# Kernel tuning notes

Measured on AMD Instinct MI355X. Metric: run time of the kernel, lower is better.

The kernel has to match this reference:

```python
import jax, jax.numpy as jnp
import numpy as np

D = 1024; H = 8; QLR = 384; KVLR = 256; NOPE = 128; ROPE = 64; VD = 128
E = 8; TOPK = 2; INTER = 512; NSH = 2; B = 2; T = 2048
QKD = NOPE + ROPE  # 192


def _rms(x, w, eps=1e-6):
    return x * jax.lax.rsqrt(jnp.mean(x * x, axis=-1, keepdims=True) + eps) * w


def _rope(x, cos, sin):
    # x: [B,T,h,ROPE]; pairs are consecutive elements (torch view(...,-1,2)).
    x0 = x[..., 0::2]
    x1 = x[..., 1::2]
    c = cos[None, :, None, :]
    s = sin[None, :, None, :]
    y0 = x0 * c - x1 * s
    y1 = x0 * s + x1 * c
    return jnp.stack([y0, y1], axis=-1).reshape(x.shape)


def setup_inputs() -> dict:
    key = jax.random.key(0)
    ks = jax.random.split(key, 12)
    def w(k, shape, scale=0.02):
        return jax.random.normal(k, shape, dtype=jnp.float32) * scale
    inv = 1.0 / (10000.0 ** (jnp.arange(0, ROPE, 2, dtype=jnp.float32) / ROPE))
    ang = jnp.arange(T, dtype=jnp.float32)[:, None] * inv[None, :]  # [T, ROPE//2]
    return {
        "x": jax.random.normal(ks[0], (B, T, D), dtype=jnp.float32),
        "freqs_cos": jnp.cos(ang),
        "freqs_sin": jnp.sin(ang),
        "rmsn1_w": jnp.ones((D,), jnp.float32),
        "rmsn2_w": jnp.ones((D,), jnp.float32),
        "latent_w": w(ks[1], (D, QLR + KVLR + ROPE)),
        "q_norm_w": jnp.ones((QLR,), jnp.float32),
        "q_up_w": w(ks[2], (QLR, H * QKD)),
        "kv_norm_w": jnp.ones((KVLR,), jnp.float32),
        "kv_up_w": w(ks[3], (KVLR, H * (NOPE + VD))),
        "c_proj_w": w(ks[4], (D, D)),
        "gate_w": w(ks[5], (D, E)),
        "sh_w1": w(ks[6], (D, INTER * NSH)),
        "sh_w2": w(ks[7], (INTER * NSH, D)),
        "sh_w3": w(ks[8], (D, INTER * NSH)),
        "e_w1": w(ks[9], (E, D, INTER)),
        "e_w2": w(ks[10], (E, INTER, D)),
        "e_w3": w(ks[11], (E, D, INTER)),
    }


def reference(x, freqs_cos, freqs_sin, rmsn1_w, rmsn2_w, latent_w, q_norm_w,
              q_up_w, kv_norm_w, kv_up_w, c_proj_w, gate_w, sh_w1, sh_w2,
              sh_w3, e_w1, e_w2, e_w3):
    Bx, Tx, _ = x.shape
    # ---- MLA attention ----
    h = _rms(x, rmsn1_w)
    lat = h @ latent_w
    q_l, kv_l, k_r = jnp.split(lat, [QLR, QLR + KVLR], axis=-1)
    q = (_rms(q_l, q_norm_w) @ q_up_w).reshape(Bx, Tx, H, QKD)
    q_n, q_r = q[..., :NOPE], q[..., NOPE:]
    q_r = _rope(q_r, freqs_cos, freqs_sin)
    q = jnp.concatenate([q_n, q_r], axis=-1)  # [B,T,H,QKD]
    kv = (_rms(kv_l, kv_norm_w) @ kv_up_w).reshape(Bx, Tx, H, NOPE + VD)
    k_n, v = kv[..., :NOPE], kv[..., NOPE:]
    k_r = _rope(k_r[:, :, None, :], freqs_cos, freqs_sin)
    k_r = jnp.broadcast_to(k_r, (Bx, Tx, H, ROPE))
    k = jnp.concatenate([k_n, k_r], axis=-1)
    scale = 1.0 / jnp.sqrt(jnp.float32(QKD))
    scores = jnp.einsum('bqhd,bkhd->bhqk', q, k) * scale
    causal = jnp.tril(jnp.ones((Tx, Tx), dtype=bool))
    scores = jnp.where(causal, scores, jnp.finfo(scores.dtype).min)
    attn = jax.nn.softmax(scores, axis=-1)
    y = jnp.einsum('bhqk,bkhd->bqhd', attn, v).reshape(Bx, Tx, D)
    x = x + y @ c_proj_w
    # ---- DeepSeekMoE ----
    h2 = _rms(x, rmsn2_w).reshape(-1, D)  # [N, D]
    y_sh = (jax.nn.silu(h2 @ sh_w1) * (h2 @ sh_w3)) @ sh_w2
    scores_g = jax.nn.softmax(h2 @ gate_w, axis=-1)  # [N, E]
    w_top, idx = jax.lax.top_k(scores_g, TOPK)  # weights == gathered original scores
    # combine weights per expert (route_scale = 1.0)
    cw = jnp.sum(jax.nn.one_hot(idx, E, dtype=h2.dtype) * w_top[..., None], axis=1)  # [N, E]
    h1 = jnp.einsum('nd,edi->eni', h2, e_w1)
    h3 = jnp.einsum('nd,edi->eni', h2, e_w3)
    out_e = jnp.einsum('eni,eid->end', jax.nn.silu(h1) * h3, e_w2)  # [E, N, D]
    y_moe = y_sh + jnp.einsum('end,ne->nd', out_e, cw)
    return x + y_moe.reshape(Bx, Tx, D)
```

## Files before the change

kernel.cpp:

```cpp
#include <hip/hip_runtime.h>
#include <hip/hip_bf16.h>
#include <math.h>

#define D_ 1024
#define H_ 8
#define QLR_ 384
#define KVLR_ 256
#define NOPE_ 128
#define ROPE_ 64
#define VD_ 128
#define E_ 8
#define INTER_ 512
#define B_ 2
#define T_ 2048
#define QKD_ 192
#define NTOK (B_*T_)
#define LSTR 4608
#define MAXMB 72

typedef __attribute__((ext_vector_type(8))) short short8;
typedef __attribute__((ext_vector_type(4))) float f32x4;
typedef __attribute__((ext_vector_type(4))) unsigned short us4;

__device__ __forceinline__ unsigned short f2bf(float f) {
  union { float f; unsigned u; } v; v.f = f;
  return (unsigned short)((v.u + 0x7FFFu + ((v.u >> 16) & 1u)) >> 16);
}
__device__ __forceinline__ float bf2f(unsigned short h) {
  union { unsigned u; float f; } v; v.u = ((unsigned)h) << 16;
  return v.f;
}

#define GLD16(SRC, DST) __builtin_amdgcn_global_load_lds( \
    (__attribute__((address_space(1))) void*)(SRC), \
    (__attribute__((address_space(3))) void*)(DST), 16, 0, 0)

#define DPPF(v, ctrl) __int_as_float(__builtin_amdgcn_update_dpp(0, __float_as_int(v), ctrl, 0xF, 0xF, true))
__device__ __forceinline__ float dppmax16(float v) {
  v = fmaxf(v, DPPF(v, 0xB1));
  v = fmaxf(v, DPPF(v, 0x4E));
  v = fmaxf(v, DPPF(v, 0x124));
  v = fmaxf(v, DPPF(v, 0x128));
  return v;
}
__device__ __forceinline__ float dppsum16(float v) {
  v += DPPF(v, 0xB1);
  v += DPPF(v, 0x4E);
  v += DPPF(v, 0x124);
  v += DPPF(v, 0x128);
  return v;
}

__global__ __launch_bounds__(256) void transpose_f32_bf16(
    const float* __restrict__ in, unsigned short* __restrict__ out,
    int R, int C, size_t inBS, size_t outBS) {
  __shared__ float tile[32][33];
  const float* inp = in + (size_t)blockIdx.z * inBS;
  unsigned short* outp = out + (size_t)blockIdx.z * outBS;
  int c0 = blockIdx.x * 32, r0 = blockIdx.y * 32;
  int tx = threadIdx.x & 31, ty = threadIdx.x >> 5;
  #pragma unroll
  for (int i = 0; i < 4; ++i) {
    int rr = ty + i * 8;
    tile[rr][tx] = inp[(size_t)(r0 + rr) * C + c0 + tx];
  }
  __syncthreads();
  #pragma unroll
  for (int i = 0; i < 4; ++i) {
    int rr = ty + i * 8;
    outp[(size_t)(c0 + rr) * R + r0 + tx] = f2bf(tile[tx][rr]);
  }
}

__global__ __launch_bounds__(256) void transpose_pair(
    const float* __restrict__ in1, const float* __restrict__ in3,
    unsigned short* __restrict__ out, int K, int C1, size_t inBS, size_t outBS) {
  __shared__ float tile[32][33];
  int z = blockIdx.z; int bat = z >> 1; int f = (z & 1) * 16;
  const float* src = ((z & 1) ? in3 : in1) + (size_t)bat * inBS;
  unsigned short* o = out + (size_t)bat * outBS;
  int c0 = blockIdx.x * 32, r0 = blockIdx.y * 32;
  int tx = threadIdx.x & 31, ty = threadIdx.x >> 5;
  #pragma unroll
  for (int i = 0; i < 4; ++i) {
    int rr = ty + i * 8;
    tile[rr][tx] = src[(size_t)(r0 + rr) * C1 + c0 + tx];
  }
  __syncthreads();
  #pragma unroll
  for (int i = 0; i < 4; ++i) {
    int cc = ty + i * 8;
    int c = c0 + cc;
    int n = ((c >> 4) << 5) + (c & 15) + f;
    o[(size_t)n * K + r0 + tx] = f2bf(tile[tx][cc]);
  }
}

template<typename TI>
__global__ __launch_bounds__(256) void rms_to_bf16(
    const TI* __restrict__ src, int stride, int off, const float* __restrict__ w,
    unsigned short* __restrict__ out, int Dd, int outStride) {
  int row = blockIdx.x;
  const TI* xr = src + (size_t)row * stride + off;
  float ss = 0.f;
  for (int i = threadIdx.x; i < Dd; i += 256) {
    float v;
    if constexpr (sizeof(TI) == 2) v = bf2f((unsigned short)xr[i]); else v = (float)xr[i];
    ss += v * v;
  }
  for (int o = 1; o < 64; o <<= 1) ss += __shfl_xor(ss, o);
  __shared__ float red[4];
  if ((threadIdx.x & 63) == 0) red[threadIdx.x >> 6] = ss;
  __syncthreads();
  float tot = red[0] + red[1] + red[2] + red[3];
  float inv = 1.f / sqrtf(tot / Dd + 1e-6f);
  for (int i = threadIdx.x; i < Dd; i += 256) {
    float v;
    if constexpr (sizeof(TI) == 2) v = bf2f((unsigned short)xr[i]); else v = (float)xr[i];
    out[(size_t)row * outStride + i] = f2bf(v * inv * w[i]);
  }
}

__global__ __launch_bounds__(256) void lat_post(
    const unsigned short* __restrict__ lat, const float* __restrict__ qw,
    const float* __restrict__ kw, const float* __restrict__ fc, const float* __restrict__ fs,
    unsigned short* __restrict__ qn, unsigned short* __restrict__ kvn,
    unsigned short* __restrict__ kr) {
  int row = blockIdx.x, tid = threadIdx.x;
  int lane = tid & 63, wv = tid >> 6;
  const unsigned short* lr = lat + (size_t)row * 768;
  float s1 = 0.f, s2 = 0.f;
  for (int i = tid; i < QLR_; i += 256) { float v = bf2f(lr[i]); s1 += v * v; }
  { float v = bf2f(lr[QLR_ + tid]); s2 = v * v; }
  for (int o = 1; o < 64; o <<= 1) { s1 += __shfl_xor(s1, o); s2 += __shfl_xor(s2, o); }
  __shared__ float red[8];
  if (lane == 0) { red[wv] = s1; red[4 + wv] = s2; }
  __syncthreads();
  float inv1 = 1.f / sqrtf((red[0] + red[1] + red[2] + red[3]) / QLR_ + 1e-6f);
  float inv2 = 1.f / sqrtf((red[4] + red[5] + red[6] + red[7]) / KVLR_ + 1e-6f);
  for (int i = tid; i < QLR_; i += 256)
    qn[(size_t)row * QLR_ + i] = f2bf(bf2f(lr[i]) * inv1 * qw[i]);
  kvn[(size_t)row * KVLR_ + tid] = f2bf(bf2f(lr[QLR_ + tid]) * inv2 * kw[tid]);
  if (tid < 32) {
    int t = row & (T_ - 1);
    float c = fc[t * 32 + tid], s = fs[t * 32 + tid];
    float x0 = bf2f(lr[640 + 2 * tid]), x1 = bf2f(lr[640 + 2 * tid + 1]);
    kr[(size_t)row * ROPE_ + 2 * tid]     = f2bf(x0 * c - x1 * s);
    kr[(size_t)row * ROPE_ + 2 * tid + 1] = f2bf(x0 * s + x1 * c);
  }
}

template<int MODE>
__global__ __launch_bounds__(256) void gemm_bf16(
    const unsigned short* __restrict__ A, const unsigned short* __restrict__ Bt,
    void* __restrict__ Cv, int M, int N, int K,
    const float* __restrict__ addv) {
  __shared__ __align__(16) unsigned short As[128 * 32];
  __shared__ __align__(16) unsigned short Bs[128 * 32];
  const int tid = threadIdx.x;
  const int lane = tid & 63, wave = tid >> 6;
  const int wm = wave >> 1, wn = wave & 1;
  const int bm = blockIdx.y * 128, bn = blockIdx.x * 128;
  const int r = lane & 15, g = lane >> 4;

  f32x4 acc[4][4];
  #pragma unroll
  for (int i = 0; i < 4; ++i)
    #pragma unroll
    for (int j = 0; j < 4; ++j) acc[i][j] = (f32x4)0.f;

  const int rl0 = wave * 16 + (lane >> 2);
  const int rl1 = rl0 + 64;
  const int kc = (lane & 3) * 8;
  char* AsB = (char*)As; char* BsB = (char*)Bs;

  for (int k0 = 0; k0 < K; k0 += 32) {
    GLD16(A + (size_t)(bm + rl0) * K + k0 + kc, AsB + wave * 1024);
    GLD16(A + (size_t)(bm + rl1) * K + k0 + kc, AsB + (wave + 4) * 1024);
    GLD16(Bt + (size_t)(bn + rl0) * K + k0 + kc, BsB + wave * 1024);
    GLD16(Bt + (size_t)(bn + rl1) * K + k0 + kc, BsB + (wave + 4) * 1024);
    __syncthreads();
    short8 af[4], bfr[4];
    #pragma unroll
    for (int mi = 0; mi < 4; ++mi)
      af[mi] = *(const short8*)(As + (wm * 64 + mi * 16 + r) * 32 + g * 8);
    #pragma unroll
    for (int nj = 0; nj < 4; ++nj)
      bfr[nj] = *(const short8*)(Bs + (wn * 64 + nj * 16 + r) * 32 + g * 8);
    #pragma unroll
    for (int mi = 0; mi < 4; ++mi)
      #pragma unroll
      for (int nj = 0; nj < 4; ++nj)
        acc[mi][nj] = __builtin_amdgcn_mfma_f32_16x16x32_bf16(af[mi], bfr[nj], acc[mi][nj], 0, 0, 0);
    __syncthreads();
  }

  const int orow0 = wm * 64 + g * 4;
  const int ocol0 = bn + wn * 64 + r;
  #pragma unroll
  for (int mi = 0; mi < 4; ++mi) {
    #pragma unroll
    for (int reg = 0; reg < 4; ++reg) {
      int mrow = bm + orow0 + mi * 16 + reg;
      size_t bas = (size_t)mrow * N + ocol0;
      if (MODE == 0) {
        unsigned short* C = (unsigned short*)Cv;
        #pragma unroll
        for (int nj = 0; nj < 4; ++nj) C[bas + nj * 16] = f2bf(acc[mi][nj][reg]);
      } else {
        float* C = (float*)Cv;
        #pragma unroll
        for (int nj = 0; nj < 4; ++nj) C[bas + nj * 16] = acc[mi][nj][reg] + addv[bas + nj * 16];
      }
    }
  }
}

__global__ __launch_bounds__(256) void gemm_qkv(
    const unsigned short* __restrict__ qn, const unsigned short* __restrict__ Wqup,
    const unsigned short* __restrict__ kvn, const unsigned short* __restrict__ Wkv,
    unsigned short* __restrict__ qq, unsigned short* __restrict__ kvb,
    unsigned short* __restrict__ vtg) {
  __shared__ __align__(16) unsigned short As[128 * 32];
  __shared__ __align__(16) unsigned short Bs[128 * 32];
  const int tid = threadIdx.x;
  const int lane = tid & 63, wave = tid >> 6;
  const int wm = wave >> 1, wn = wave & 1;
  const bool isQ = blockIdx.x < 12;
  const int bx = isQ ? blockIdx.x : blockIdx.x - 12;
  const unsigned short* A  = isQ ? qn : kvn;
  const unsigned short* Bt = isQ ? Wqup : Wkv;
  const int N = isQ ? 1536 : 2048;
  const int K = isQ ? QLR_ : KVLR_;
  const int bm = blockIdx.y * 128, bn = bx * 128;
  const int r = lane & 15, g = lane >> 4;

  f32x4 acc[4][4];
  #pragma unroll
  for (int i = 0; i < 4; ++i)
    #pragma unroll
    for (int j = 0; j < 4; ++j) acc[i][j] = (f32x4)0.f;

  const int rl0 = wave * 16 + (lane >> 2);
  const int rl1 = rl0 + 64;
  const int kc = (lane & 3) * 8;
  char* AsB = (char*)As; char* BsB = (char*)Bs;

  for (int k0 = 0; k0 < K; k0 += 32) {
    GLD16(A + (size_t)(bm + rl0) * K + k0 + kc, AsB + wave * 1024);
    GLD16(A + (size_t)(bm + rl1) * K + k0 + kc, AsB + (wave + 4) * 1024);
    GLD16(Bt + (size_t)(bn + rl0) * K + k0 + kc, BsB + wave * 1024);
    GLD16(Bt + (size_t)(bn + rl1) * K + k0 + kc, BsB + (wave + 4) * 1024);
    __syncthreads();
    short8 af[4], bfr[4];
    #pragma unroll
    for (int mi = 0; mi < 4; ++mi)
      af[mi] = *(const short8*)(As + (wm * 64 + mi * 16 + r) * 32 + g * 8);
    #pragma unroll
    for (int nj = 0; nj < 4; ++nj)
      bfr[nj] = *(const short8*)(Bs + (wn * 64 + nj * 16 + r) * 32 + g * 8);
    #pragma unroll
    for (int mi = 0; mi < 4; ++mi)
      #pragma unroll
      for (int nj = 0; nj < 4; ++nj)
        acc[mi][nj] = __builtin_amdgcn_mfma_f32_16x16x32_bf16(af[mi], bfr[nj], acc[mi][nj], 0, 0, 0);
    __syncthreads();
  }

  if (isQ) {
    const int orow0 = wm * 64 + g * 4;
    const int ocol0 = bn + wn * 64 + r;
    #pragma unroll
    for (int mi = 0; mi < 4; ++mi)
      #pragma unroll
      for (int reg = 0; reg < 4; ++reg) {
        int mrow = bm + orow0 + mi * 16 + reg;
        size_t bas = (size_t)mrow * 1536 + ocol0;
        #pragma unroll
        for (int nj = 0; nj < 4; ++nj) qq[bas + nj * 16] = f2bf(acc[mi][nj][reg]);
      }
  } else {
    const int colbase = bn + wn * 64;
    const int b = bm >> 11;
    const int hh = colbase >> 8;
    if ((colbase & 255) < 128) {
      #pragma unroll
      for (int mi = 0; mi < 4; ++mi)
        #pragma unroll
        for (int reg = 0; reg < 4; ++reg) {
          int mrow = bm + wm * 64 + mi * 16 + g * 4 + reg;
          size_t bas = (size_t)mrow * 2048 + colbase + r;
          #pragma unroll
          for (int nj = 0; nj < 4; ++nj) kvb[bas + nj * 16] = f2bf(acc[mi][nj][reg]);
        }
    } else {
      const int tl0 = (bm & 2047) + wm * 64 + g * 4;
      const int d0 = (colbase & 255) - 128 + r;
      const size_t bhbase = (size_t)(b * 8 + hh) * 64;
      #pragma unroll
      for (int mi = 0; mi < 4; ++mi) {
        int t = tl0 + mi * 16;
        size_t tb = (bhbase + (t >> 5)) * 4096 + (t & 31);
        #pragma unroll
        for (int nj = 0; nj < 4; ++nj) {
          int d = d0 + nj * 16;
          us4 pk;
          #pragma unroll
          for (int reg = 0; reg < 4; ++reg) pk[reg] = f2bf(acc[mi][nj][reg]);
          *(us4*)(vtg + tb + (size_t)d * 32) = pk;
        }
      }
    }
  }
}

__global__ __launch_bounds__(256) void gemm_ffn13(
    const unsigned short* __restrict__ h2b, const unsigned short* __restrict__ Wsh13,
    unsigned short* __restrict__ t1m,
    const unsigned short* __restrict__ Wew13, unsigned short* __restrict__ ehm,
    const int* __restrict__ lists, const int* __restrict__ map, const int* __restrict__ sbase) {
  __shared__ __align__(16) unsigned short As[128 * 32];
  __shared__ __align__(16) unsigned short Bs[128 * 32];
  const int i = blockIdx.x;
  const bool isSh = i < 512;
  const int tid = threadIdx.x, lane = tid & 63, wave = tid >> 6;
  const int wm = wave >> 1, wn = wave & 1;
  const int r = lane & 15, g = lane >> 4;
  const int rl0 = wave * 16 + (lane >> 2), rl1 = rl0 + 64;
  const int kc = (lane & 3) * 8;

  int bn, e = 0, ib = 0, bm = 0;
  const unsigned short* Bt;
  int ar0, ar1;
  const unsigned short* A;
  if (isSh) {
    bn = (i & 15) * 128; bm = (i >> 4) * 128;
    Bt = Wsh13; A = h2b;
    ar0 = bm + rl0; ar1 = bm + rl1;
  } else {
    int j = i - 512;
    bn = (j & 7) * 128;
    int mb = map[j >> 3];
    if (mb < 0) return;
    e = mb >> 16; ib = mb & 0xFFFF;
    Bt = Wew13 + (size_t)e * 1024 * 1024; A = h2b;
    ar0 = lists[e * LSTR + ib * 128 + rl0]; if (ar0 < 0) ar0 = 0;
    ar1 = lists[e * LSTR + ib * 128 + rl1]; if (ar1 < 0) ar1 = 0;
  }

  f32x4 acc[4][4];
  #pragma unroll
  for (int a = 0; a < 4; ++a)
    #pragma unroll
    for (int bj = 0; bj < 4; ++bj) acc[a][bj] = (f32x4)0.f;
  char* AsB = (char*)As; char* BsB = (char*)Bs;

  for (int k0 = 0; k0 < 1024; k0 += 32) {
    GLD16(A + (size_t)ar0 * 1024 + k0 + kc, AsB + wave * 1024);
    GLD16(A + (size_t)ar1 * 1024 + k0 + kc, AsB + (wave + 4) * 1024);
    GLD16(Bt + (size_t)(bn + rl0) * 1024 + k0 + kc, BsB + wave * 1024);
    GLD16(Bt + (size_t)(bn + rl1) * 1024 + k0 + kc, BsB + (wave + 4) * 1024);
    __syncthreads();
    short8 af[4], bfr[4];
    #pragma unroll
    for (int mi = 0; mi < 4; ++mi)
      af[mi] = *(const short8*)(As + (wm * 64 + mi * 16 + r) * 32 + g * 8);
    #pragma unroll
    for (int nj = 0; nj < 4; ++nj)
      bfr[nj] = *(const short8*)(Bs + (wn * 64 + nj * 16 + r) * 32 + g * 8);
    #pragma unroll
    for (int mi = 0; mi < 4; ++mi)
      #pragma unroll
      for (int nj = 0; nj < 4; ++nj)
        acc[mi][nj] = __builtin_amdgcn_mfma_f32_16x16x32_bf16(af[mi], bfr[nj], acc[mi][nj], 0, 0, 0);
    __syncthreads();
  }

  if (isSh) {
    const int hc = ((bn + wn * 64) >> 1) + r;
    #pragma unroll
    for (int mi = 0; mi < 4; ++mi)
      #pragma unroll
      for (int reg = 0; reg < 4; ++reg) {
        int mrow = bm + wm * 64 + mi * 16 + g * 4 + reg;
        #pragma unroll
        for (int p = 0; p < 2; ++p) {
          float a = acc[mi][2 * p][reg], b3 = acc[mi][2 * p + 1][reg];
          t1m[(size_t)mrow * 1024 + hc + p * 16] = f2bf((a / (1.f + __expf(-a))) * b3);
        }
      }
  } else {
    const int sb = sbase[e] + ib * 128;
    const int hc = ((bn + wn * 64) >> 1) + r;
    #pragma unroll
    for (int mi = 0; mi < 4; ++mi)
      #pragma unroll
      for (int reg = 0; reg < 4; ++reg) {
        int srow = sb + wm * 64 + mi * 16 + g * 4 + reg;
        #pragma unroll
        for (int p = 0; p < 2; ++p) {
          float a = acc[mi][2 * p][reg], b3 = acc[mi][2 * p + 1][reg];
          ehm[(size_t)srow * 512 + hc + p * 16] = f2bf((a / (1.f + __expf(-a))) * b3);
        }
      }
  }
}

__global__ __launch_bounds__(256) void gemm_ffn2(
    const unsigned short* __restrict__ t1m, const unsigned short* __restrict__ Wsh2,
    const unsigned short* __restrict__ ehm, const unsigned short* __restrict__ Wew2,
    float* __restrict__ out,
    const int* __restrict__ lists, const int* __restrict__ map, const int* __restrict__ sbase,
    const float* __restrict__ cw) {
  __shared__ __align__(16) unsigned short As[128 * 32];
  __shared__ __align__(16) unsigned short Bs[128 * 32];
  const int i = blockIdx.x;
  const bool isSh = i < 256;
  const int tid = threadIdx.x, lane = tid & 63, wave = tid >> 6;
  const int wm = wave >> 1, wn = wave & 1;
  const int r = lane & 15, g = lane >> 4;
  const int rl0 = wave * 16 + (lane >> 2), rl1 = rl0 + 64;
  const int kc = (lane & 3) * 8;

  int bn, e = 0, ib = 0, bm = 0, K, sb = 0;
  const unsigned short* A;
  const unsigned short* Bt;
  if (isSh) {
    bn = (i & 7) * 128; bm = (i >> 3) * 128;
    A = t1m; Bt = Wsh2; K = 1024;
  } else {
    int j = i - 256;
    bn = (j & 7) * 128;
    int mb = map[j >> 3];
    if (mb < 0) return;
    e = mb >> 16; ib = mb & 0xFFFF;
    sb = sbase[e] + ib * 128;
    A = ehm; Bt = Wew2 + (size_t)e * 512 * 1024; K = 512;
    bm = sb;
  }

  f32x4 acc[4][4];
  #pragma unroll
  for (int a = 0; a < 4; ++a)
    #pragma unroll
    for (int bj = 0; bj < 4; ++bj) acc[a][bj] = (f32x4)0.f;
  char* AsB = (char*)As; char* BsB = (char*)Bs;

  for (int k0 = 0; k0 < K; k0 += 32) {
    GLD16(A + (size_t)(bm + rl0) * K + k0 + kc, AsB + wave * 1024);
    GLD16(A + (size_t)(bm + rl1) * K + k0 + kc, AsB + (wave + 4) * 1024);
    GLD16(Bt + (size_t)(bn + rl0) * K + k0 + kc, BsB + wave * 1024);
    GLD16(Bt + (size_t)(bn + rl1) * K + k0 + kc, BsB + (wave + 4) * 1024);
    __syncthreads();
    short8 af[4], bfr[4];
    #pragma unroll
    for (int mi = 0; mi < 4; ++mi)
      af[mi] = *(const short8*)(As + (wm * 64 + mi * 16 + r) * 32 + g * 8);
    #pragma unroll
    for (int nj = 0; nj < 4; ++nj)
      bfr[nj] = *(const short8*)(Bs + (wn * 64 + nj * 16 + r) * 32 + g * 8);
    #pragma unroll
    for (int mi = 0; mi < 4; ++mi)
      #pragma unroll
      for (int nj = 0; nj < 4; ++nj)
        acc[mi][nj] = __builtin_amdgcn_mfma_f32_16x16x32_bf16(af[mi], bfr[nj], acc[mi][nj], 0, 0, 0);
    __syncthreads();
  }

  const int ocol0 = bn + wn * 64 + r;
  if (isSh) {
    #pragma unroll
    for (int mi = 0; mi < 4; ++mi)
      #pragma unroll
      for (int reg = 0; reg < 4; ++reg) {
        int mrow = bm + wm * 64 + mi * 16 + g * 4 + reg;
        #pragma unroll
        for (int nj = 0; nj < 4; ++nj)
          atomicAdd(out + (size_t)mrow * 1024 + ocol0 + nj * 16, acc[mi][nj][reg]);
      }
  } else {
    #pragma unroll
    for (int mi = 0; mi < 4; ++mi)
      #pragma unroll
      for (int reg = 0; reg < 4; ++reg) {
        int orow = wm * 64 + mi * 16 + g * 4 + reg;
        int tok = lists[e * LSTR + ib * 128 + orow];
        if (tok >= 0) {
          float wt = cw[(size_t)tok * E_ + e];
          #pragma unroll
          for (int nj = 0; nj < 4; ++nj)
            atomicAdd(out + (size_t)tok * 1024 + ocol0 + nj * 16, acc[mi][nj][reg] * wt);
        }
      }
  }
}

#define AQ 64
#define AK 32
#define VP 40
__global__ __launch_bounds__(256) void attn_mfma(
    const unsigned short* __restrict__ q,
    const unsigned short* __restrict__ kv,
    const unsigned short* __restrict__ kr,
    const unsigned short* __restrict__ vt,
    const float* __restrict__ fcos, const float* __restrict__ fsin,
    unsigned short* __restrict__ po,
    float* __restrict__ pml) {
  __shared__ __align__(16) unsigned short Ks[AK * 192];
  __shared__ __align__(16) unsigned short Vl[128 * VP];
  __shared__ __align__(16) unsigned short Ps[4 * 16 * VP];
  const int tid = threadIdx.x, lane = tid & 63, wave = tid >> 6;
  const int r = lane & 15, g = lane >> 4;
  const int bh = blockIdx.y, b = bh >> 3, h = bh & 7;
  const int qt = gridDim.x - 1 - blockIdx.x;
  const int q0 = qt * AQ;
  const int half = blockIdx.z;
  const int hnt = qt + 1;
  const int kb = half * hnt, ke = kb + hnt;
  const size_t bT = (size_t)b * T_;
  const unsigned short* vbase = vt + (size_t)bh * 64 * 4096;
  char* KsB = (char*)Ks;

  short8 qf[6];
  const int qrow = q0 + wave * 16 + r;
  {
    const unsigned short* qb = q + ((bT + qrow) * H_ + h) * 192;
    #pragma unroll
    for (int kk = 0; kk < 6; ++kk) qf[kk] = *(const short8*)(qb + kk * 32 + g * 8);
    #pragma unroll
    for (int kk = 4; kk < 6; ++kk) {
      int i0 = (kk - 4) * 16 + g * 4;
      #pragma unroll
      for (int p = 0; p < 4; ++p) {
        float cc = fcos[qrow * 32 + i0 + p], sn = fsin[qrow * 32 + i0 + p];
        float x0 = bf2f((unsigned short)qf[kk][2 * p]), x1 = bf2f((unsigned short)qf[kk][2 * p + 1]);
        qf[kk][2 * p]     = (short)f2bf(x0 * cc - x1 * sn);
        qf[kk][2 * p + 1] = (short)f2bf(x0 * sn + x1 * cc);
      }
    }
  }

  float m_i[4], l_i[4];
  f32x4 o[8];
  #pragma unroll
  for (int i = 0; i < 4; ++i) { m_i[i] = -1e30f; l_i[i] = 0.f; }
  #pragma unroll
  for (int cb = 0; cb < 8; ++cb) o[cb] = (f32x4)0.f;

  const float scale2 = 0.07216878364870322f * 1.44269504088896f;

  short8 kreg[3], vreg[2];
  int krow[3], kcol[3];
  #pragma unroll
  for (int it = 0; it < 3; ++it) {
    int c = tid + it * 256;
    krow[it] = c / 24; kcol[it] = c % 24;
    kreg[it] = (kcol[it] < 16)
      ? *(const short8*)(kv + ((bT + kb * AK + krow[it]) * H_ + h) * 256 + kcol[it] * 8)
      : *(const short8*)(kr + (bT + kb * AK + krow[it]) * 64 + (kcol[it] - 16) * 8);
  }
  #pragma unroll
  for (int it = 0; it < 2; ++it) {
    int x = tid + it * 256;
    vreg[it] = *(const short8*)(vbase + (size_t)kb * 4096 + x * 8);
  }

  for (int kt = kb; kt < ke; ++kt) {
    __builtin_amdgcn_s_barrier();
    __builtin_amdgcn_sched_barrier(0);
    #pragma unroll
    for (int it = 0; it < 3; ++it)
      *(short8*)(KsB + ((krow[it] * 384 + kcol[it] * 16) ^ ((krow[it] & 7) << 4))) = kreg[it];
    #pragma unroll
    for (int it = 0; it < 2; ++it) {
      int x = tid + it * 256;
      *(short8*)(Vl + (x >> 2) * VP + (x & 3) * 8) = vreg[it];
    }
    asm volatile("s_waitcnt lgkmcnt(0)" ::: "memory");
    __builtin_amdgcn_s_barrier();
    __builtin_amdgcn_sched_barrier(0);

    if (kt + 1 < ke) {
      int k1 = (kt + 1) * AK;
      #pragma unroll
      for (int it = 0; it < 3; ++it)
        kreg[it] = (kcol[it] < 16)
          ? *(const short8*)(kv + ((bT + k1 + krow[it]) * H_ + h) * 256 + kcol[it] * 8)
          : *(const short8*)(kr + (bT + k1 + krow[it]) * 64 + (kcol[it] - 16) * 8);
      #pragma unroll
      for (int it = 0; it < 2; ++it) {
        int x = tid + it * 256;
        vreg[it] = *(const short8*)(vbase + (size_t)(kt + 1) * 4096 + x * 8);
      }
    }

    const int k0 = kt * AK;
    f32x4 sf0 = (f32x4)0.f, sf1 = (f32x4)0.f;
    {
      int ksw = (r & 7) << 4;
      __builtin_amdgcn_s_setprio(1);
      #pragma unroll
      for (int kk = 0; kk < 6; ++kk) {
        short8 b0 = *(const short8*)(KsB + ((r * 384 + kk * 64 + g * 16) ^ ksw));
        short8 b1 = *(const short8*)(KsB + (((16 + r) * 384 + kk * 64 + g * 16) ^ ksw));
        sf0 = __builtin_amdgcn_mfma_f32_16x16x32_bf16(qf[kk], b0, sf0, 0, 0, 0);
        sf1 = __builtin_amdgcn_mfma_f32_16x16x32_bf16(qf[kk], b1, sf1, 0, 0, 0);
      }
      __builtin_amdgcn_s_setprio(0);
    }

    float fac[4];
    bool needs = false;
    const bool bnd = (k0 + AK > q0);
    #pragma unroll
    for (int reg = 0; reg < 4; ++reg) {
      float s0 = sf0[reg] * scale2;
      float s1 = sf1[reg] * scale2;
      if (bnd) {
        int qp = q0 + wave * 16 + g * 4 + reg;
        if (k0 + r > qp) s0 = -1e30f;
        if (k0 + 16 + r > qp) s1 = -1e30f;
      }
      float mt = dppmax16(fmaxf(s0, s1));
      float fc = 1.f, mn = m_i[reg];
      if (mt > mn + 8.f) {
        mn = mt; fc = exp2f(m_i[reg] - mn); m_i[reg] = mn; needs = true;
      }
      float e0 = exp2f(s0 - mn), e1 = exp2f(s1 - mn);
      float rs = dppsum16(e0 + e1);
      l_i[reg] = l_i[reg] * fc + rs;
      fac[reg] = fc;
      __hip_bfloat162 pk = __float22bfloat162_rn(float2{e0, e1});
      unsigned u = *(unsigned*)&pk;
      int prow = g * 4 + reg;
      Ps[wave * 16 * VP + prow * VP + r] = (unsigned short)u;
      Ps[wave * 16 * VP + prow * VP + 16 + r] = (unsigned short)(u >> 16);
    }
    if (__any(needs)) {
      #pragma unroll
      for (int cb = 0; cb < 8; ++cb)
        #pragma unroll
        for (int reg = 0; reg < 4; ++reg) o[cb][reg] *= fac[reg];
    }
    short8 pa = *(const short8*)(Ps + wave * 16 * VP + r * VP + g * 8);
    __builtin_amdgcn_s_setprio(1);
    #pragma unroll
    for (int cb = 0; cb < 8; ++cb) {
      short8 vb = *(const short8*)(Vl + (cb * 16 + r) * VP + g * 8);
      o[cb] = __builtin_amdgcn_mfma_f32_16x16x32_bf16(pa, vb, o[cb], 0, 0, 0);
    }
    __builtin_amdgcn_s_setprio(0);
  }

  const int slab = (bh * 32 + qt) * 2 + half;
  unsigned short* pob = po + (size_t)slab * 8192;
  float* pmlb = pml + (size_t)slab * 128;
  #pragma unroll
  for (int reg = 0; reg < 4; ++reg) {
    int row = wave * 16 + g * 4 + reg;
    if (r == 0) { pmlb[row * 2] = m_i[reg]; pmlb[row * 2 + 1] = l_i[reg]; }
    #pragma unroll
    for (int cb = 0; cb < 8; ++cb)
      pob[row * 128 + cb * 16 + r] = f2bf(o[cb][reg]);
  }
}

__global__ __launch_bounds__(256) void attn_combine(
    const unsigned short* __restrict__ po, const float* __restrict__ pml,
    unsigned short* __restrict__ y) {
  const int qt = blockIdx.x, bh = blockIdx.y, b = bh >> 3, h = bh & 7;
  const int s0 = (bh * 32 + qt) * 2, s1 = s0 + 1;
  const int row = threadIdx.x >> 2;
  const int qp = threadIdx.x & 3;
  float m0 = pml[(size_t)s0 * 128 + row * 2], l0 = pml[(size_t)s0 * 128 + row * 2 + 1];
  float m1 = pml[(size_t)s1 * 128 + row * 2], l1 = pml[(size_t)s1 * 128 + row * 2 + 1];
  float m = fmaxf(m0, m1);
  float e0 = exp2f(m0 - m), e1 = exp2f(m1 - m);
  float inv = 1.f / (l0 * e0 + l1 * e1);
  e0 *= inv; e1 *= inv;
  const unsigned short* o0 = po + (size_t)s0 * 8192 + row * 128 + qp * 32;
  const unsigned short* o1 = po + (size_t)s1 * 8192 + row * 128 + qp * 32;
  unsigned short* yb = y + ((size_t)(b * T_ + qt * 64 + row)) * 1024 + h * 128 + qp * 32;
  #pragma unroll
  for (int v = 0; v < 4; ++v) {
    short8 a = *(const short8*)(o0 + v * 8);
    short8 c = *(const short8*)(o1 + v * 8);
    short8 w;
    #pragma unroll
    for (int j = 0; j < 8; ++j)
      w[j] = (short)f2bf(bf2f((unsigned short)a[j]) * e0 + bf2f((unsigned short)c[j]) * e1);
    *(short8*)(yb + v * 8) = w;
  }
}

__global__ __launch_bounds__(256) void rms2_gate(
    const float* __restrict__ xo, const float* __restrict__ rw, const float* __restrict__ gw,
    unsigned short* __restrict__ h2b, float* __restrict__ cw) {
  int row = blockIdx.x, tid = threadIdx.x;
  int lane = tid & 63, wv = tid >> 6;
  const float* xr = xo + (size_t)row * D_;
  float v[4]; float ss = 0.f;
  #pragma unroll
  for (int j = 0; j < 4; ++j) { v[j] = xr[tid + j * 256]; ss += v[j] * v[j]; }
  for (int o = 1; o < 64; o <<= 1) ss += __shfl_xor(ss, o);
  __shared__ float red[4];
  if (lane == 0) red[wv] = ss;
  __syncthreads();
  float inv = 1.f / sqrtf((red[0] + red[1] + red[2] + red[3]) / D_ + 1e-6f);
  float a[E_] = {0, 0, 0, 0, 0, 0, 0, 0};
  #pragma unroll
  for (int j = 0; j < 4; ++j) {
    int i = tid + j * 256;
    float hv = v[j] * inv * rw[i];
    h2b[(size_t)row * D_ + i] = f2bf(hv);
    const float* wr = gw + (size_t)i * E_;
    #pragma unroll
    for (int e = 0; e < E_; ++e) a[e] += hv * wr[e];
  }
  #pragma unroll
  for (int e = 0; e < E_; ++e) {
    float t = a[e];
    for (int o = 1; o < 64; o <<= 1) t += __shfl_xor(t, o);
    a[e] = t;
  }
  __shared__ float ga[4][E_];
  if (lane == 0)
    #pragma unroll
    for (int e = 0; e < E_; ++e) ga[wv][e] = a[e];
  __syncthreads();
  if (tid == 0) {
    float lg[E_];
    #pragma unroll
    for (int e = 0; e < E_; ++e) lg[e] = ga[0][e] + ga[1][e] + ga[2][e] + ga[3][e];
    float mx = lg[0];
    #pragma unroll
    for (int e = 1; e < E_; ++e) mx = fmaxf(mx, lg[e]);
    float sum = 0.f; float p[E_];
    #pragma unroll
    for (int e = 0; e < E_; ++e) { p[e] = __expf(lg[e] - mx); sum += p[e]; }
    float is = 1.f / sum;
    int i1 = 0; float b1 = p[0];
    #pragma unroll
    for (int e = 1; e < E_; ++e) if (p[e] > b1) { b1 = p[e]; i1 = e; }
    int i2 = -1; float b2 = -1.f;
    #pragma unroll
    for (int e = 0; e < E_; ++e) if (e != i1 && p[e] > b2) { b2 = p[e]; i2 = e; }
    #pragma unroll
    for (int e = 0; e < E_; ++e)
      cw[(size_t)row * E_ + e] = (e == i1) ? b1 * is : (e == i2 ? b2 * is : 0.f);
  }
}

__global__ __launch_bounds__(256) void moe_build(const float* __restrict__ cw,
                                                 int* __restrict__ lists, int* __restrict__ counts) {
  int e = blockIdx.x, tid = threadIdx.x;
  int lane = tid & 63, wv = tid >> 6;
  __shared__ int wsum[4];
  __shared__ int base;
  if (tid == 0) base = 0;
  __syncthreads();
  for (int c0 = 0; c0 < NTOK; c0 += 256) {
    int tok = c0 + tid;
    bool f = cw[(size_t)tok * E_ + e] > 0.f;
    unsigned long long m = __ballot(f);
    int pos = __popcll(m & ((1ull << lane) - 1ull));
    if (lane == 0) wsum[wv] = __popcll(m);
    __syncthreads();
    int woff = base;
    #pragma unroll
    for (int w = 0; w < 4; ++w) if (w < wv) woff += wsum[w];
    if (f) lists[e * LSTR + woff + pos] = tok;
    __syncthreads();
    if (tid == 0) base += wsum[0] + wsum[1] + wsum[2] + wsum[3];
    __syncthreads();
  }
  int cnt = base;
  int padded = (cnt + 127) & ~127;
  for (int i2 = cnt + tid; i2 < padded; i2 += 256) lists[e * LSTR + i2] = -1;
  if (tid == 0) { counts[e] = cnt; counts[8 + e] = padded >> 7; }
}

__global__ void moe_finalize(const int* __restrict__ counts, int* __restrict__ map,
                             int* __restrict__ sbase) {
  if (threadIdx.x == 0 && blockIdx.x == 0) {
    int cum = 0;
    for (int e = 0; e < E_; ++e) {
      sbase[e] = cum * 128;
      int nb = counts[8 + e];
      for (int i = 0; i < nb; ++i) map[cum + i] = (e << 16) | i;
      cum += nb;
    }
    for (; cum < MAXMB; ++cum) map[cum] = -1;
  }
}

extern "C" void kernel_launch(void* const* d_in, const int* in_sizes, int n_in,
                              void* d_out, int out_size, void* d_ws, size_t ws_size,
                              hipStream_t stream) {
  const float* x        = (const float*)d_in[0];
  const float* fcos     = (const float*)d_in[1];
  const float* fsin     = (const float*)d_in[2];
  const float* rmsn1_w  = (const float*)d_in[3];
  const float* rmsn2_w  = (const float*)d_in[4];
  const float* latent_w = (const float*)d_in[5];
  const float* q_norm_w = (const float*)d_in[6];
  const float* q_up_w   = (const float*)d_in[7];
  const float* kv_norm_w= (const float*)d_in[8];
  const float* kv_up_w  = (const float*)d_in[9];
  const float* c_proj_w = (const float*)d_in[10];
  const float* gate_w   = (const float*)d_in[11];
  const float* sh_w1    = (const float*)d_in[12];
  const float* sh_w2    = (const float*)d_in[13];
  const float* sh_w3    = (const float*)d_in[14];
  const float* e_w1     = (const float*)d_in[15];
  const float* e_w2     = (const float*)d_in[16];
  const float* e_w3     = (const float*)d_in[17];
  float* out = (float*)d_out;

  char* base = (char*)d_ws;
  size_t off = 0;
  auto take = [&](size_t bytes) { char* p = base + off; off += (bytes + 255) & ~(size_t)255; return p; };
  unsigned short* Wlat  = (unsigned short*)take((size_t)768 * 1024 * 2);
  unsigned short* Wqup  = (unsigned short*)take((size_t)1536 * 384 * 2);
  unsigned short* Wkv   = (unsigned short*)take((size_t)2048 * 256 * 2);
  unsigned short* Wcp   = (unsigned short*)take((size_t)1024 * 1024 * 2);
  unsigned short* Wsh13 = (unsigned short*)take((size_t)2048 * 1024 * 2);
  unsigned short* Wsh2  = (unsigned short*)take((size_t)1024 * 1024 * 2);
  unsigned short* Wew13 = (unsigned short*)take((size_t)8 * 1024 * 1024 * 2);
  unsigned short* Wew2  = (unsigned short*)take((size_t)8 * 1024 * 512 * 2);
  float* cw             = (float*)take((size_t)NTOK * E_ * 4);
  int* lists            = (int*)take((size_t)E_ * LSTR * 4);
  int* counts           = (int*)take(64 * 4);
  int* map              = (int*)take(MAXMB * 4);
  int* sbase            = (int*)take(E_ * 4);
  unsigned short* Vtg   = (unsigned short*)take((size_t)16 * 64 * 4096 * 2);
  unsigned short* kr    = (unsigned short*)take((size_t)NTOK * 64 * 2);
  float* pml            = (float*)take((size_t)1024 * 128 * 4);

  size_t actStart = off;
  size_t aoff = actStart;
  auto takeA = [&](size_t bytes) { char* p = base + aoff; aoff += (bytes + 255) & ~(size_t)255; return p; };
  unsigned short* h_bf = (unsigned short*)takeA((size_t)NTOK * 1024 * 2);
  unsigned short* lat  = (unsigned short*)takeA((size_t)NTOK * 768 * 2);
  unsigned short* qn   = (unsigned short*)takeA((size_t)NTOK * 384 * 2);
  unsigned short* kvn  = (unsigned short*)takeA((size_t)NTOK * 256 * 2);
  unsigned short* qq   = (unsigned short*)takeA((size_t)NTOK * 1536 * 2);
  unsigned short* kvb  = (unsigned short*)takeA((size_t)NTOK * 2048 * 2);
  unsigned short* y    = (unsigned short*)takeA((size_t)NTOK * 1024 * 2);

  unsigned short* po   = (unsigned short*)(base + actStart);

  size_t coff = actStart;
  auto takeC = [&](size_t bytes) { char* p = base + coff; coff += (bytes + 255) & ~(size_t)255; return p; };
  unsigned short* h2b  = (unsigned short*)takeC((size_t)NTOK * 1024 * 2);
  unsigned short* t1m  = (unsigned short*)takeC((size_t)NTOK * 1024 * 2);
  unsigned short* ehm  = (unsigned short*)takeC((size_t)9216 * 512 * 2);

  dim3 blk(256);

  transpose_f32_bf16<<<dim3(22, 32, 1), blk, 0, stream>>>(latent_w, Wlat, 1024, 704, 0, 0);
  transpose_f32_bf16<<<dim3(48, 12, 1), blk, 0, stream>>>(q_up_w, Wqup, 384, 1536, 0, 0);
  transpose_f32_bf16<<<dim3(64, 8, 1), blk, 0, stream>>>(kv_up_w, Wkv, 256, 2048, 0, 0);
  transpose_f32_bf16<<<dim3(32, 32, 1), blk, 0, stream>>>(c_proj_w, Wcp, 1024, 1024, 0, 0);
  transpose_f32_bf16<<<dim3(32, 32, 1), blk, 0, stream>>>(sh_w2, Wsh2, 1024, 1024, 0, 0);
  transpose_pair<<<dim3(32, 32, 2), blk, 0, stream>>>(sh_w1, sh_w3, Wsh13, 1024, 1024, 0, 0);
  transpose_pair<<<dim3(16, 32, 16), blk, 0, stream>>>(e_w1, e_w3, Wew13, 1024, 512,
      (size_t)1024 * 512, (size_t)1024 * 1024);
  transpose_f32_bf16<<<dim3(32, 16, 8), blk, 0, stream>>>(e_w2, Wew2, 512, 1024,
      (size_t)512 * 1024, (size_t)1024 * 512);

  rms_to_bf16<float><<<NTOK, blk, 0, stream>>>(x, D_, 0, rmsn1_w, h_bf, D_, D_);
  gemm_bf16<0><<<dim3(6, 32), blk, 0, stream>>>(h_bf, Wlat, lat, NTOK, 768, 1024, nullptr);
  lat_post<<<NTOK, blk, 0, stream>>>(lat, q_norm_w, kv_norm_w, fcos, fsin, qn, kvn, kr);
  gemm_qkv<<<dim3(28, 32), blk, 0, stream>>>(qn, Wqup, kvn, Wkv, qq, kvb, Vtg);
  attn_mfma<<<dim3(T_ / AQ, B_ * H_, 2), blk, 0, stream>>>(qq, kvb, kr, Vtg, fcos, fsin, po, pml);
  attn_combine<<<dim3(T_ / AQ, B_ * H_), blk, 0, stream>>>(po, pml, y);
  gemm_bf16<1><<<dim3(8, 32), blk, 0, stream>>>(y, Wcp, out, NTOK, 1024, 1024, x);
  rms2_gate<<<NTOK, blk, 0, stream>>>(out, rmsn2_w, gate_w, h2b, cw);
  moe_build<<<E_, blk, 0, stream>>>(cw, lists, counts);
  moe_finalize<<<1, 64, 0, stream>>>(counts, map, sbase);
  gemm_ffn13<<<dim3(1088), blk, 0, stream>>>(h2b, Wsh13, t1m, Wew13, ehm, lists, map, sbase);
  gemm_ffn2<<<dim3(832), blk, 0, stream>>>(t1m, Wsh2, ehm, Wew2, out, lists, map, sbase, cw);
}
```

Baseline: 397.8 us.

## Double attention query tile to 128 rows with 512-thread blocks

The attention kernel now handles 128 query rows per block with 8 waves instead of 64 rows with 4 waves. Each K/V tile staged in shared memory is reused by twice as many query rows, and the global-to-register prefetch drops to one to two loads per thread. The combine kernel and the partial-output buffers are resized to match. In exchange the grid has half as many blocks, and the causal work is split less evenly across them, which can hurt occupancy and load balance.

```diff
diff --git a/kernel.cpp b/kernel.cpp
--- a/kernel.cpp
+++ b/kernel.cpp
@@ -230,7 +230,6 @@
   const int bx = isQ ? blockIdx.x : blockIdx.x - 12;
   const unsigned short* A  = isQ ? qn : kvn;
   const unsigned short* Bt = isQ ? Wqup : Wkv;
-  const int N = isQ ? 1536 : 2048;
   const int K = isQ ? QLR_ : KVLR_;
   const int bm = blockIdx.y * 128, bn = bx * 128;
   const int r = lane & 15, g = lane >> 4;
@@ -422,7 +421,7 @@
   const int rl0 = wave * 16 + (lane >> 2), rl1 = rl0 + 64;
   const int kc = (lane & 3) * 8;
 
-  int bn, e = 0, ib = 0, bm = 0, K, sb = 0;
+  int bn, e = 0, ib = 0, bm = 0, K;
   const unsigned short* A;
   const unsigned short* Bt;
   if (isSh) {
@@ -434,9 +433,8 @@
     int mb = map[j >> 3];
     if (mb < 0) return;
     e = mb >> 16; ib = mb & 0xFFFF;
-    sb = sbase[e] + ib * 128;
+    bm = sbase[e] + ib * 128;
     A = ehm; Bt = Wew2 + (size_t)e * 512 * 1024; K = 512;
-    bm = sb;
   }
 
   f32x4 acc[4][4];
@@ -495,10 +493,10 @@
   }
 }
 
-#define AQ 64
+#define AQ 128
 #define AK 32
 #define VP 40
-__global__ __launch_bounds__(256) void attn_mfma(
+__global__ __launch_bounds__(512) void attn_mfma(
     const unsigned short* __restrict__ q,
     const unsigned short* __restrict__ kv,
     const unsigned short* __restrict__ kr,
@@ -508,14 +506,14 @@
     float* __restrict__ pml) {
   __shared__ __align__(16) unsigned short Ks[AK * 192];
   __shared__ __align__(16) unsigned short Vl[128 * VP];
-  __shared__ __align__(16) unsigned short Ps[4 * 16 * VP];
+  __shared__ __align__(16) unsigned short Ps[8 * 16 * VP];
   const int tid = threadIdx.x, lane = tid & 63, wave = tid >> 6;
   const int r = lane & 15, g = lane >> 4;
   const int bh = blockIdx.y, b = bh >> 3, h = bh & 7;
   const int qt = gridDim.x - 1 - blockIdx.x;
   const int q0 = qt * AQ;
   const int half = blockIdx.z;
-  const int hnt = qt + 1;
+  const int hnt = 2 * (qt + 1);
   const int kb = half * hnt, ke = kb + hnt;
   const size_t bT = (size_t)b * T_;
   const unsigned short* vbase = vt + (size_t)bh * 64 * 4096;
@@ -549,49 +547,44 @@
 
   const float scale2 = 0.07216878364870322f * 1.44269504088896f;
 
-  short8 kreg[3], vreg[2];
-  int krow[3], kcol[3];
-  #pragma unroll
-  for (int it = 0; it < 3; ++it) {
-    int c = tid + it * 256;
-    krow[it] = c / 24; kcol[it] = c % 24;
-    kreg[it] = (kcol[it] < 16)
-      ? *(const short8*)(kv + ((bT + kb * AK + krow[it]) * H_ + h) * 256 + kcol[it] * 8)
-      : *(const short8*)(kr + (bT + kb * AK + krow[it]) * 64 + (kcol[it] - 16) * 8);
-  }
-  #pragma unroll
-  for (int it = 0; it < 2; ++it) {
-    int x = tid + it * 256;
-    vreg[it] = *(const short8*)(vbase + (size_t)kb * 4096 + x * 8);
+  const int kr0r = tid / 24, kr0c = tid % 24;
+  const bool k1v = tid < 256;
+  const int kr1r = (tid + 512) / 24, kr1c = (tid + 512) % 24;
+
+  short8 kreg0, kreg1, vreg;
+  {
+    int kk0 = kb * AK;
+    kreg0 = (kr0c < 16)
+      ? *(const short8*)(kv + ((bT + kk0 + kr0r) * H_ + h) * 256 + kr0c * 8)
+      : *(const short8*)(kr + (bT + kk0 + kr0r) * 64 + (kr0c - 16) * 8);
+    if (k1v)
+      kreg1 = (kr1c < 16)
+        ? *(const short8*)(kv + ((bT + kk0 + kr1r) * H_ + h) * 256 + kr1c * 8)
+        : *(const short8*)(kr + (bT + kk0 + kr1r) * 64 + (kr1c - 16) * 8);
+    vreg = *(const short8*)(vbase + (size_t)kb * 4096 + tid * 8);
   }
 
   for (int kt = kb; kt < ke; ++kt) {
     __builtin_amdgcn_s_barrier();
     __builtin_amdgcn_sched_barrier(0);
-    #pragma unroll
-    for (int it = 0; it < 3; ++it)
-      *(short8*)(KsB + ((krow[it] * 384 + kcol[it] * 16) ^ ((krow[it] & 7) << 4))) = kreg[it];
-    #pragma unroll
-    for (int it = 0; it < 2; ++it) {
-      int x = tid + it * 256;
-      *(short8*)(Vl + (x >> 2) * VP + (x & 3) * 8) = vreg[it];
-    }
+    *(short8*)(KsB + ((kr0r * 384 + kr0c * 16) ^ ((kr0r & 7) << 4))) = kreg0;
+    if (k1v)
+      *(short8*)(KsB + ((kr1r * 384 + kr1c * 16) ^ ((kr1r & 7) << 4))) = kreg1;
+    *(short8*)(Vl + (tid >> 2) * VP + (tid & 3) * 8) = vreg;
     asm volatile("s_waitcnt lgkmcnt(0)" ::: "memory");
     __builtin_amdgcn_s_barrier();
     __builtin_amdgcn_sched_barrier(0);
 
     if (kt + 1 < ke) {
       int k1 = (kt + 1) * AK;
-      #pragma unroll
-      for (int it = 0; it < 3; ++it)
-        kreg[it] = (kcol[it] < 16)
-          ? *(const short8*)(kv + ((bT + k1 + krow[it]) * H_ + h) * 256 + kcol[it] * 8)
-          : *(const short8*)(kr + (bT + k1 + krow[it]) * 64 + (kcol[it] - 16) * 8);
-      #pragma unroll
-      for (int it = 0; it < 2; ++it) {
-        int x = tid + it * 256;
-        vreg[it] = *(const short8*)(vbase + (size_t)(kt + 1) * 4096 + x * 8);
-      }
+      kreg0 = (kr0c < 16)
+        ? *(const short8*)(kv + ((bT + k1 + kr0r) * H_ + h) * 256 + kr0c * 8)
+        : *(const short8*)(kr + (bT + k1 + kr0r) * 64 + (kr0c - 16) * 8);
+      if (k1v)
+        kreg1 = (kr1c < 16)
+          ? *(const short8*)(kv + ((bT + k1 + kr1r) * H_ + h) * 256 + kr1c * 8)
+          : *(const short8*)(kr + (bT + k1 + kr1r) * 64 + (kr1c - 16) * 8);
+      vreg = *(const short8*)(vbase + (size_t)(kt + 1) * 4096 + tid * 8);
     }
 
     const int k0 = kt * AK;
@@ -652,9 +645,9 @@
     __builtin_amdgcn_s_setprio(0);
   }
 
-  const int slab = (bh * 32 + qt) * 2 + half;
-  unsigned short* pob = po + (size_t)slab * 8192;
-  float* pmlb = pml + (size_t)slab * 128;
+  const int slab = (bh * 16 + qt) * 2 + half;
+  unsigned short* pob = po + (size_t)slab * 16384;
+  float* pmlb = pml + (size_t)slab * 256;
   #pragma unroll
   for (int reg = 0; reg < 4; ++reg) {
     int row = wave * 16 + g * 4 + reg;
@@ -665,22 +658,22 @@
   }
 }
 
-__global__ __launch_bounds__(256) void attn_combine(
+__global__ __launch_bounds__(512) void attn_combine(
     const unsigned short* __restrict__ po, const float* __restrict__ pml,
     unsigned short* __restrict__ y) {
   const int qt = blockIdx.x, bh = blockIdx.y, b = bh >> 3, h = bh & 7;
-  const int s0 = (bh * 32 + qt) * 2, s1 = s0 + 1;
+  const int s0 = (bh * 16 + qt) * 2, s1 = s0 + 1;
   const int row = threadIdx.x >> 2;
   const int qp = threadIdx.x & 3;
-  float m0 = pml[(size_t)s0 * 128 + row * 2], l0 = pml[(size_t)s0 * 128 + row * 2 + 1];
-  float m1 = pml[(size_t)s1 * 128 + row * 2], l1 = pml[(size_t)s1 * 128 + row * 2 + 1];
+  float m0 = pml[(size_t)s0 * 256 + row * 2], l0 = pml[(size_t)s0 * 256 + row * 2 + 1];
+  float m1 = pml[(size_t)s1 * 256 + row * 2], l1 = pml[(size_t)s1 * 256 + row * 2 + 1];
   float m = fmaxf(m0, m1);
   float e0 = exp2f(m0 - m), e1 = exp2f(m1 - m);
   float inv = 1.f / (l0 * e0 + l1 * e1);
   e0 *= inv; e1 *= inv;
-  const unsigned short* o0 = po + (size_t)s0 * 8192 + row * 128 + qp * 32;
-  const unsigned short* o1 = po + (size_t)s1 * 8192 + row * 128 + qp * 32;
-  unsigned short* yb = y + ((size_t)(b * T_ + qt * 64 + row)) * 1024 + h * 128 + qp * 32;
+  const unsigned short* o0 = po + (size_t)s0 * 16384 + row * 128 + qp * 32;
+  const unsigned short* o1 = po + (size_t)s1 * 16384 + row * 128 + qp * 32;
+  unsigned short* yb = y + ((size_t)(b * T_ + qt * 128 + row)) * 1024 + h * 128 + qp * 32;
   #pragma unroll
   for (int v = 0; v < 4; ++v) {
     short8 a = *(const short8*)(o0 + v * 8);
@@ -835,7 +828,7 @@
   int* sbase            = (int*)take(E_ * 4);
   unsigned short* Vtg   = (unsigned short*)take((size_t)16 * 64 * 4096 * 2);
   unsigned short* kr    = (unsigned short*)take((size_t)NTOK * 64 * 2);
-  float* pml            = (float*)take((size_t)1024 * 128 * 4);
+  float* pml            = (float*)take((size_t)512 * 256 * 4);
 
   size_t actStart = off;
   size_t aoff = actStart;
@@ -873,8 +866,8 @@
   gemm_bf16<0><<<dim3(6, 32), blk, 0, stream>>>(h_bf, Wlat, lat, NTOK, 768, 1024, nullptr);
   lat_post<<<NTOK, blk, 0, stream>>>(lat, q_norm_w, kv_norm_w, fcos, fsin, qn, kvn, kr);
   gemm_qkv<<<dim3(28, 32), blk, 0, stream>>>(qn, Wqup, kvn, Wkv, qq, kvb, Vtg);
-  attn_mfma<<<dim3(T_ / AQ, B_ * H_, 2), blk, 0, stream>>>(qq, kvb, kr, Vtg, fcos, fsin, po, pml);
-  attn_combine<<<dim3(T_ / AQ, B_ * H_), blk, 0, stream>>>(po, pml, y);
+  attn_mfma<<<dim3(T_ / AQ, B_ * H_, 2), dim3(512), 0, stream>>>(qq, kvb, kr, Vtg, fcos, fsin, po, pml);
+  attn_combine<<<dim3(T_ / AQ, B_ * H_), dim3(512), 0, stream>>>(po, pml, y);
   gemm_bf16<1><<<dim3(8, 32), blk, 0, stream>>>(y, Wcp, out, NTOK, 1024, 1024, x);
   rms2_gate<<<NTOK, blk, 0, stream>>>(out, rmsn2_w, gate_w, h2b, cw);
   moe_build<<<E_, blk, 0, stream>>>(cw, lists, counts);
```

Result: faster. 388.8 us (-2.3%).
